# Kernel tuning notes

Measured on AMD Instinct MI355X. Metric: run time of the kernel, lower is better.

Reference implementation:

```python
import jax, jax.numpy as jnp
import numpy as np

NQ = 10
C64 = jnp.complex64

# ---- gate matrices (built from traced fp32 params) ----

def u3(t, p, d):
    c = jnp.cos(t * 0.5).astype(C64)
    s = jnp.sin(t * 0.5).astype(C64)
    ep = jnp.exp(1j * p.astype(C64))
    ed = jnp.exp(1j * d.astype(C64))
    return jnp.stack([jnp.stack([c, -ed * s]), jnp.stack([ep * s, ep * ed * c])])

def ry(t):
    c = jnp.cos(t * 0.5).astype(C64)
    s = jnp.sin(t * 0.5).astype(C64)
    return jnp.stack([jnp.stack([c, -s]), jnp.stack([s, c])])

def rz(t):
    e = jnp.exp(-0.5j * t.astype(C64))
    ep = jnp.exp(0.5j * t.astype(C64))
    return jnp.diag(jnp.stack([e, ep]))

def rx(t):
    c = jnp.cos(t * 0.5).astype(C64)
    s = jnp.sin(t * 0.5).astype(C64)
    return jnp.stack([jnp.stack([c, -1j * s]), jnp.stack([-1j * s, c])])

def crz(t):
    one = jnp.ones((), C64)
    return jnp.diag(jnp.stack([one, one, jnp.exp(-0.5j * t.astype(C64)), jnp.exp(0.5j * t.astype(C64))]))

def crx(t):
    return jnp.eye(4, dtype=C64).at[2:, 2:].set(rx(t))

X = jnp.array([[0, 1], [1, 0]], dtype=C64)
CNOT = jnp.array([[1, 0, 0, 0], [0, 1, 0, 0], [0, 0, 0, 1], [0, 0, 1, 0]], dtype=C64)

# ---- gate application on state of shape (B, 2,...,2) ----

def ap1(st, U, w):
    ax = 1 + w
    s = jnp.moveaxis(st, ax, -1)
    s = s @ U.T
    return jnp.moveaxis(s, -1, ax)

def ap2(st, U, a, b):
    s = jnp.moveaxis(st, (1 + a, 1 + b), (-2, -1))
    sh = s.shape
    s = s.reshape(sh[:-2] + (4,)) @ U.T
    return jnp.moveaxis(s.reshape(sh), (-2, -1), (1 + a, 1 + b))

def conv_block(st, w, a, b):
    st = ap1(st, u3(w[0], w[1], w[2]), a)
    st = ap1(st, u3(w[3], w[4], w[5]), b)
    st = ap2(st, CNOT, a, b)
    st = ap1(st, ry(w[6]), a)
    st = ap1(st, rz(w[7]), b)
    st = ap2(st, CNOT, b, a)
    st = ap1(st, ry(w[8]), a)
    st = ap2(st, CNOT, a, b)
    st = ap1(st, u3(w[9], w[10], w[11]), a)
    st = ap1(st, u3(w[12], w[13], w[14]), b)
    return st

def pool_block(st, p, c, t):
    st = ap2(st, crz(p[0]), c, t)
    st = ap1(st, X, c)
    st = ap2(st, crx(p[1]), c, t)
    return st

def zexp(st, w):
    p = jnp.abs(st) ** 2  # fp32
    axes = tuple(ax for ax in range(1, NQ + 1) if ax != 1 + w)
    pz = p.sum(axis=axes)  # (B, 2)
    return pz[:, 0] - pz[:, 1]


def setup_inputs() -> dict:
    key = jax.random.key(0)
    ks = jax.random.split(key, 6)
    two_pi = 2.0 * np.pi
    return {
        "x": jax.random.normal(ks[0], (16384, 1024), dtype=jnp.float32),
        "weights_conv1": jax.random.uniform(ks[1], (10, 15), jnp.float32) * two_pi,
        "weights_conv2": jax.random.uniform(ks[2], (4, 15), jnp.float32) * two_pi,
        "weights_pool1": jax.random.uniform(ks[3], (5, 2), jnp.float32) * two_pi,
        "weights_pool2": jax.random.uniform(ks[4], (2, 2), jnp.float32) * two_pi,
        "weights_fc": jax.random.uniform(ks[5], (3,), jnp.float32) * two_pi,
    }


def reference(x, weights_conv1, weights_conv2, weights_pool1, weights_pool2, weights_fc):
    B = x.shape[0]
    # AmplitudeEmbedding with normalize=True (input already 1024-dim, no padding)
    nrm = jnp.linalg.norm(x, axis=1, keepdims=True)
    st = (x / nrm).astype(C64).reshape((B,) + (2,) * NQ)
    # conv layer 1: even pairs, odd pairs, wraparound (0, 9) reusing row 7
    for i in range(0, NQ, 2):
        st = conv_block(st, weights_conv1[i], i, i + 1)
    for i in range(1, NQ - 1, 2):
        st = conv_block(st, weights_conv1[i], i, i + 1)
    st = conv_block(st, weights_conv1[7], 0, NQ - 1)
    # pool layer 1
    for idx, i in enumerate(range(0, NQ, 2)):
        st = pool_block(st, weights_pool1[idx], i + 1, i)
    # conv layer 2 (stride-2 wires)
    for idx, i in enumerate(range(0, NQ - 2, 2)):
        st = conv_block(st, weights_conv2[idx], i, i + 2)
    # pool layer 2
    for idx, i in enumerate(range(0, NQ - 2, 4)):
        st = pool_block(st, weights_pool2[idx], i + 2, i)
    # fully-connected entanglers + RX rotations
    st = ap2(st, CNOT, 0, 4)
    st = ap2(st, CNOT, 2, 4)
    st = ap2(st, CNOT, 4, 0)
    st = ap1(st, rx(weights_fc[0]), 0)
    st = ap1(st, rx(weights_fc[1]), 2)
    st = ap1(st, rx(weights_fc[2]), 4)
    return jnp.stack([zexp(st, 0), zexp(st, 2)], axis=-1)  # (B, 2)
```

## Files before the change

kernel.cpp:

```cpp
#include <hip/hip_runtime.h>


typedef _Float16 f16;
typedef f16 f16x8 __attribute__((ext_vector_type(8)));
typedef f16 f16x4 __attribute__((ext_vector_type(4)));
typedef f16 f16x2 __attribute__((ext_vector_type(2)));
typedef float f32x4 __attribute__((ext_vector_type(4)));

__device__ inline float2 cmul(float2 a, float2 b) {
    return make_float2(a.x * b.x - a.y * b.y, a.x * b.y + a.y * b.x);
}
__device__ inline float2 cadd(float2 a, float2 b) {
    return make_float2(a.x + b.x, a.y + b.y);
}

struct M2 { float2 m[4]; };

__device__ inline M2 m2_u3(float t, float p, float d) {
    float c = cosf(0.5f * t), s = sinf(0.5f * t);
    float2 ep = make_float2(cosf(p), sinf(p));
    float2 ed = make_float2(cosf(d), sinf(d));
    M2 U;
    U.m[0] = make_float2(c, 0.f);
    U.m[1] = make_float2(-ed.x * s, -ed.y * s);
    U.m[2] = make_float2(ep.x * s, ep.y * s);
    float2 epd = cmul(ep, ed);
    U.m[3] = make_float2(epd.x * c, epd.y * c);
    return U;
}
__device__ inline M2 m2_ry(float t) {
    float c = cosf(0.5f * t), s = sinf(0.5f * t);
    M2 U;
    U.m[0] = make_float2(c, 0.f);  U.m[1] = make_float2(-s, 0.f);
    U.m[2] = make_float2(s, 0.f);  U.m[3] = make_float2(c, 0.f);
    return U;
}
__device__ inline M2 m2_rz(float t) {
    float c = cosf(0.5f * t), s = sinf(0.5f * t);
    M2 U;
    U.m[0] = make_float2(c, -s); U.m[1] = make_float2(0.f, 0.f);
    U.m[2] = make_float2(0.f, 0.f); U.m[3] = make_float2(c, s);
    return U;
}
__device__ inline M2 m2_rx(float t) {
    float c = cosf(0.5f * t), s = sinf(0.5f * t);
    M2 U;
    U.m[0] = make_float2(c, 0.f);   U.m[1] = make_float2(0.f, -s);
    U.m[2] = make_float2(0.f, -s);  U.m[3] = make_float2(c, 0.f);
    return U;
}

__device__ inline void ap2x2(float2& x, float2& y, const M2& U) {
    float2 nx = cadd(cmul(U.m[0], x), cmul(U.m[1], y));
    float2 ny = cadd(cmul(U.m[2], x), cmul(U.m[3], y));
    x = nx; y = ny;
}
__device__ inline void apA(float2 v[4], const M2& U) { ap2x2(v[0], v[2], U); ap2x2(v[1], v[3], U); }
__device__ inline void apB(float2 v[4], const M2& U) { ap2x2(v[0], v[1], U); ap2x2(v[2], v[3], U); }
__device__ inline void swapv(float2& a, float2& b) { float2 t = a; a = b; b = t; }

__device__ inline void conv_col(const float* w, float2 v[4]) {
    apA(v, m2_u3(w[0], w[1], w[2]));
    apB(v, m2_u3(w[3], w[4], w[5]));
    swapv(v[2], v[3]);
    apA(v, m2_ry(w[6]));
    apB(v, m2_rz(w[7]));
    swapv(v[1], v[3]);
    apA(v, m2_ry(w[8]));
    swapv(v[2], v[3]);
    apA(v, m2_u3(w[9], w[10], w[11]));
    apB(v, m2_u3(w[12], w[13], w[14]));
}
__device__ inline void pool_col(const float* p, float2 v[4]) {
    {
        float c = cosf(0.5f * p[0]), s = sinf(0.5f * p[0]);
        v[2] = cmul(v[2], make_float2(c, -s));
        v[3] = cmul(v[3], make_float2(c, s));
    }
    swapv(v[0], v[2]); swapv(v[1], v[3]);
    {
        M2 U = m2_rx(p[1]);
        ap2x2(v[2], v[3], U);
    }
}

__global__ void build_gates(const float* wc1, const float* wc2,
                            const float* wp1, const float* wp2,
                            const float* wfc, int2* gp, float2* gm) {
    const int t = threadIdx.x;
    const int n = t >> 2, c = t & 3;
    if (blockIdx.x != 0 || n >= 27) return;

    float2 v[4];
    for (int i = 0; i < 4; i++) v[i] = make_float2(0.f, 0.f);
    v[c] = make_float2(1.f, 0.f);

    int a, b;
    if (n < 5)        { int i = 2*n;       a = i;   b = i+1; conv_col(wc1 + 15*i, v); }
    else if (n < 9)   { int i = 2*(n-5)+1; a = i;   b = i+1; conv_col(wc1 + 15*i, v); }
    else if (n == 9)  { a = 0; b = 9;      conv_col(wc1 + 105, v); }
    else if (n < 15)  { int idx = n-10, i = 2*idx; a = i+1; b = i; pool_col(wp1 + 2*idx, v); }
    else if (n < 19)  { int idx = n-15, i = 2*idx; a = i; b = i+2; conv_col(wc2 + 15*idx, v); }
    else if (n == 19) { a = 2; b = 0;      pool_col(wp2 + 0, v); }
    else if (n == 20) { a = 6; b = 4;      pool_col(wp2 + 2, v); }
    else if (n <= 23) {
        a = (n == 21) ? 0 : (n == 22) ? 2 : 4;
        b = (n == 23) ? 0 : 4;
        swapv(v[2], v[3]);
    } else {
        a = (n == 24) ? 0 : (n == 25) ? 2 : 4;
        b = a + 1;
        apA(v, m2_rx(wfc[n - 24]));
    }
    if (c == 0) gp[n] = make_int2(9 - a, 9 - b);
    for (int i = 0; i < 4; i++) gm[n * 16 + i * 4 + c] = v[i];
}

#define SIM_BLOCKS 512
#define NORM_BLOCKS 2048

__global__ __launch_bounds__(256) void prep(const float* __restrict__ X,
                                            const int2* __restrict__ gp,
                                            const float2* __restrict__ gm,
                                            float* __restrict__ nrm2,
                                            f16* __restrict__ Xh,
                                            f16* __restrict__ BTh,
                                            float* __restrict__ out) {
    __shared__ float2 st[2][1025];
    const int bid = blockIdx.x;

    if (bid >= SIM_BLOCKS) {
        const int nb = bid - SIM_BLOCKS;
        const int w = threadIdx.x >> 6, l = threadIdx.x & 63;
        if (threadIdx.x < 16) out[nb * 16 + threadIdx.x] = 1.0f;
#pragma unroll
        for (int r = 0; r < 2; r++) {
            const int row = nb * 8 + w * 2 + r;
            const float4* xr = (const float4*)(X + (size_t)row * 1024);
            float s = 0.f;
#pragma unroll
            for (int ch = 0; ch < 4; ch++) {
                float4 v = xr[ch * 64 + l];
                f16x4 h;
                h[0] = (f16)v.x; h[1] = (f16)v.y; h[2] = (f16)v.z; h[3] = (f16)v.w;
                *(f16x4*)(Xh + (size_t)row * 1024 + (ch * 64 + l) * 4) = h;
                s += v.x * v.x + v.y * v.y + v.z * v.z + v.w * v.w;
            }
#pragma unroll
            for (int off = 32; off >= 1; off >>= 1) s += __shfl_xor(s, off, 64);
            if (l == 0) nrm2[row] = s;
        }
        return;
    }

    const int sb = bid;
    const int t0 = (sb & 7) * 128 + (sb >> 3) * 2;

    for (int i = threadIdx.x; i < 1024; i += 256) {
        st[0][i] = make_float2((i == t0) ? 1.f : 0.f, 0.f);
        st[1][i] = make_float2((i == t0 + 1) ? 1.f : 0.f, 0.f);
    }
    __syncthreads();

    for (int g = 0; g < 27; g++) {
        const int2 p = gp[g];
        float2 m[16];
#pragma unroll
        for (int i = 0; i < 16; i++) m[i] = gm[g * 16 + i];
        const int p1 = p.x, p2 = p.y;
        const int lo = min(p1, p2), hi = max(p1, p2);
        const int q = threadIdx.x;
        const int m1 = (1 << lo) - 1;
        int tt = (q & m1) | ((q & ~m1) << 1);
        const int m2m = (1 << hi) - 1;
        const int i0 = (tt & m2m) | ((tt & ~m2m) << 1);
        int idx[4];
        for (int ga = 0; ga < 2; ga++)
            for (int gb = 0; gb < 2; gb++)
                idx[2 * ga + gb] = i0 | (ga << p1) | (gb << p2);
#pragma unroll
        for (int c = 0; c < 2; c++) {
            float2 v[4];
#pragma unroll
            for (int i = 0; i < 4; i++) v[i] = st[c][idx[i]];
#pragma unroll
            for (int i = 0; i < 4; i++) {
                float2 s = make_float2(0.f, 0.f);
#pragma unroll
                for (int j = 0; j < 4; j++) s = cadd(s, cmul(m[i * 4 + j], v[j]));
                st[c][idx[i]] = s;
            }
        }
        __syncthreads();
    }

    for (int s = threadIdx.x; s < 1024; s += 256) {
        const int b9 = (s >> 9) & 1, b7 = (s >> 7) & 1;
        if (b9 | b7) {
            const int grp = b9 ? b7 : 2;
            const int pos = (((s >> 8) & 1) << 7) | (s & 127);
            const int np = grp * 256 + pos;
            f16x2 re, im;
#pragma unroll
            for (int c = 0; c < 2; c++) {
                re[c] = (f16)st[c][s].x;
                im[c] = (f16)st[c][s].y;
            }
            *(f16x2*)(BTh + (size_t)np * 1024 + t0) = re;
            *(f16x2*)(BTh + (size_t)(np + 768) * 1024 + t0) = im;
        }
    }
}

__device__ __forceinline__ void glds16(const void* g, void* l) {
    __builtin_amdgcn_global_load_lds(
        (const __attribute__((address_space(1))) void*)g,
        (__attribute__((address_space(3))) void*)l, 16, 0, 0);
}

__global__ __launch_bounds__(512, 1) void gemm_mfma(const f16* __restrict__ A,
                                                    const f16* __restrict__ Bt,
                                                    const float* __restrict__ nrm2,
                                                    float* __restrict__ out) {
    __shared__ char lds[131072];
    const int tid = threadIdx.x;
    const int l = tid & 63, w = tid >> 6;
    const int wr = w >> 2, wc = w & 3;

    const int lin = blockIdx.x;
    const int xcd = lin & 7;
    const int mm = lin >> 3;
    const int rowT = xcd + 8 * (mm / 6);
    const int j = mm % 6;
    const int row0 = rowT * 256;
    const int col0 = j * 256;

    const int srow = l >> 3;
    const int kc = (l & 7) ^ (srow & 7);
    const f16* aS = A  + (size_t)(row0 + 32 * w + srow) * 1024 + kc * 8;
    const f16* bS = Bt + (size_t)(col0 + 32 * w + srow) * 1024 + kc * 8;

    int aOff[8][2], bOff[4][2];
#pragma unroll
    for (int h = 0; h < 2; h++) {
        const int cphys = (((l >> 4) + 4 * h) ^ (l & 7));
#pragma unroll
        for (int i = 0; i < 8; i++)
            aOff[i][h] = (wr * 128 + i * 16 + (l & 15)) * 128 + cphys * 16;
#pragma unroll
        for (int i = 0; i < 4; i++)
            bOff[i][h] = (wc * 64 + i * 16 + (l & 15)) * 128 + cphys * 16;
    }

    f32x4 acc[8][4];
    const f32x4 z = {0.f, 0.f, 0.f, 0.f};
#pragma unroll
    for (int i = 0; i < 8; i++)
#pragma unroll
        for (int n = 0; n < 4; n++) acc[i][n] = z;

    auto stage = [&](int t) {
        const int b = t & 1;
        char* aD = lds + b * 32768 + (32 * w) * 128;
        char* bD = lds + 65536 + b * 32768 + (32 * w) * 128;
#pragma unroll
        for (int g = 0; g < 4; ++g) {
            glds16(aS + t * 64 + g * 8 * 1024, aD + g * 1024);
            glds16(bS + t * 64 + g * 8 * 1024, bD + g * 1024);
        }
    };

    stage(0);
#pragma unroll 2
    for (int t = 0; t < 16; ++t) {
        asm volatile("s_waitcnt vmcnt(0)" ::: "memory");
        __builtin_amdgcn_s_barrier();
        if (t + 1 < 16) stage(t + 1);

        const char* aB = lds + (t & 1) * 32768;
        const char* bB = lds + 65536 + (t & 1) * 32768;
#pragma unroll
        for (int h = 0; h < 2; ++h) {
            f16x8 af[8], bf[4];
#pragma unroll
            for (int i = 0; i < 8; i++) af[i] = *(const f16x8*)(aB + aOff[i][h]);
#pragma unroll
            for (int i = 0; i < 4; i++) bf[i] = *(const f16x8*)(bB + bOff[i][h]);
            __builtin_amdgcn_s_setprio(1);
#pragma unroll
            for (int mi = 0; mi < 8; mi++)
#pragma unroll
                for (int ni = 0; ni < 4; ni++)
                    acc[mi][ni] = __builtin_amdgcn_mfma_f32_16x16x32_f16(
                        af[mi], bf[ni], acc[mi][ni], 0, 0, 0);
            __builtin_amdgcn_s_setprio(0);
        }
    }

    float c0[8][4], c1[8][4];
#pragma unroll
    for (int mi = 0; mi < 8; mi++)
#pragma unroll
        for (int rr = 0; rr < 4; rr++) { c0[mi][rr] = 0.f; c1[mi][rr] = 0.f; }
#pragma unroll
    for (int ni = 0; ni < 4; ni++) {
        const int n_glob = col0 + wc * 64 + ni * 16 + (l & 15);
        const int nm = (n_glob >= 768) ? n_glob - 768 : n_glob;
        const int grp = nm >> 8;
        const float w0 = (grp <= 1) ? 1.f : 0.f;
        const float w1 = (grp >= 1) ? 1.f : 0.f;
#pragma unroll
        for (int mi = 0; mi < 8; mi++)
#pragma unroll
            for (int rr = 0; rr < 4; rr++) {
                const float y = acc[mi][ni][rr];
                const float y2 = y * y;
                c0[mi][rr] += w0 * y2;
                c1[mi][rr] += w1 * y2;
            }
    }
#pragma unroll
    for (int off = 1; off < 16; off <<= 1)
#pragma unroll
        for (int mi = 0; mi < 8; mi++)
#pragma unroll
            for (int rr = 0; rr < 4; rr++) {
                c0[mi][rr] += __shfl_xor(c0[mi][rr], off, 64);
                c1[mi][rr] += __shfl_xor(c1[mi][rr], off, 64);
            }
    if ((l & 15) == 0) {
        const int q4 = l >> 4;
#pragma unroll
        for (int mi = 0; mi < 8; mi++)
#pragma unroll
            for (int rr = 0; rr < 4; rr++) {
                const int row = row0 + wr * 128 + mi * 16 + q4 * 4 + rr;
                const float inv = -2.0f / nrm2[row];
                atomicAdd(&out[row * 2 + 0], c0[mi][rr] * inv);
                atomicAdd(&out[row * 2 + 1], c1[mi][rr] * inv);
            }
    }
}

extern "C" void kernel_launch(void* const* d_in, const int* in_sizes, int n_in,
                              void* d_out, int out_size, void* d_ws, size_t ws_size,
                              hipStream_t stream) {
    const float* x   = (const float*)d_in[0];
    const float* wc1 = (const float*)d_in[1];
    const float* wc2 = (const float*)d_in[2];
    const float* wp1 = (const float*)d_in[3];
    const float* wp2 = (const float*)d_in[4];
    const float* wfc = (const float*)d_in[5];
    float* out = (float*)d_out;

    uintptr_t wsp = (uintptr_t)d_ws;
    int2*   gp     = (int2*)wsp;
    float2* gm     = (float2*)(wsp + 1024);
    f16*    BTh    = (f16*)(wsp + 8192);
    f16*    Xh     = (f16*)(wsp + 8192 + (3u << 20));
    float*  nrm2   = (float*)(wsp + 8192 + (35u << 20));

    build_gates<<<1, 128, 0, stream>>>(wc1, wc2, wp1, wp2, wfc, gp, gm);
    prep<<<SIM_BLOCKS + NORM_BLOCKS, 256, 0, stream>>>(x, gp, gm, nrm2, Xh, BTh, out);
    gemm_mfma<<<384, 512, 0, stream>>>(Xh, BTh, nrm2, out);
}
```

Measured before the change: 238.7 us.

## Restructure GEMM main loop into phased quadrant schedule with two blocks per CU

The GEMM inner loop is split into quadrant phases. Each phase loads a subset of A/B fragments from LDS, then issues a block of MFMAs, with s_barrier fences between phases and the global-to-LDS prefetch for the next K tile spread across them. This shrinks register fragments enough that launch_bounds can ask for 2 blocks per CU, so waves of different blocks overlap memory and math. Separately, the simulation part of prep handles 4 basis columns per block instead of 2, halving the sim block count and widening the stores. Risks include the many barriers, possible LDS limits on two 128KB blocks per CU, and register spills.

```diff
diff --git a/kernel.cpp b/kernel.cpp
--- a/kernel.cpp
+++ b/kernel.cpp
@@ -116,7 +116,7 @@
     for (int i = 0; i < 4; i++) gm[n * 16 + i * 4 + c] = v[i];
 }
 
-#define SIM_BLOCKS 512
+#define SIM_BLOCKS 256
 #define NORM_BLOCKS 2048
 
 __global__ __launch_bounds__(256) void prep(const float* __restrict__ X,
@@ -126,7 +126,7 @@
                                             f16* __restrict__ Xh,
                                             f16* __restrict__ BTh,
                                             float* __restrict__ out) {
-    __shared__ float2 st[2][1025];
+    __shared__ float2 st[4][1025];
     const int bid = blockIdx.x;
 
     if (bid >= SIM_BLOCKS) {
@@ -154,11 +154,12 @@
     }
 
     const int sb = bid;
-    const int t0 = (sb & 7) * 128 + (sb >> 3) * 2;
+    const int t0 = (sb & 7) * 128 + (sb >> 3) * 4;
 
     for (int i = threadIdx.x; i < 1024; i += 256) {
-        st[0][i] = make_float2((i == t0) ? 1.f : 0.f, 0.f);
-        st[1][i] = make_float2((i == t0 + 1) ? 1.f : 0.f, 0.f);
+#pragma unroll
+        for (int c = 0; c < 4; c++)
+            st[c][i] = make_float2((i == t0 + c) ? 1.f : 0.f, 0.f);
     }
     __syncthreads();
 
@@ -179,7 +180,7 @@
             for (int gb = 0; gb < 2; gb++)
                 idx[2 * ga + gb] = i0 | (ga << p1) | (gb << p2);
 #pragma unroll
-        for (int c = 0; c < 2; c++) {
+        for (int c = 0; c < 4; c++) {
             float2 v[4];
 #pragma unroll
             for (int i = 0; i < 4; i++) v[i] = st[c][idx[i]];
@@ -200,14 +201,14 @@
             const int grp = b9 ? b7 : 2;
             const int pos = (((s >> 8) & 1) << 7) | (s & 127);
             const int np = grp * 256 + pos;
-            f16x2 re, im;
-#pragma unroll
-            for (int c = 0; c < 2; c++) {
+            f16x4 re, im;
+#pragma unroll
+            for (int c = 0; c < 4; c++) {
                 re[c] = (f16)st[c][s].x;
                 im[c] = (f16)st[c][s].y;
             }
-            *(f16x2*)(BTh + (size_t)np * 1024 + t0) = re;
-            *(f16x2*)(BTh + (size_t)(np + 768) * 1024 + t0) = im;
+            *(f16x4*)(BTh + (size_t)np * 1024 + t0) = re;
+            *(f16x4*)(BTh + (size_t)(np + 768) * 1024 + t0) = im;
         }
     }
 }
@@ -218,7 +219,11 @@
         (__attribute__((address_space(3))) void*)l, 16, 0, 0);
 }
 
-__global__ __launch_bounds__(512, 1) void gemm_mfma(const f16* __restrict__ A,
+#define PH_BAR() do { __builtin_amdgcn_s_barrier(); \
+                      asm volatile("" ::: "memory"); } while (0)
+#define VM0()   asm volatile("s_waitcnt vmcnt(0)" ::: "memory")
+
+__global__ __launch_bounds__(512, 2) void gemm_mfma(const f16* __restrict__ A,
                                                     const f16* __restrict__ Bt,
                                                     const float* __restrict__ nrm2,
                                                     float* __restrict__ out) {
@@ -240,6 +245,19 @@
     const f16* aS = A  + (size_t)(row0 + 32 * w + srow) * 1024 + kc * 8;
     const f16* bS = Bt + (size_t)(col0 + 32 * w + srow) * 1024 + kc * 8;
 
+    auto stageA = [&](int t) {
+        char* aD = lds + (t & 1) * 32768 + (32 * w) * 128;
+#pragma unroll
+        for (int g = 0; g < 4; ++g)
+            glds16(aS + t * 64 + g * 8 * 1024, aD + g * 1024);
+    };
+    auto stageB = [&](int t) {
+        char* bD = lds + 65536 + (t & 1) * 32768 + (32 * w) * 128;
+#pragma unroll
+        for (int g = 0; g < 4; ++g)
+            glds16(bS + t * 64 + g * 8 * 1024, bD + g * 1024);
+    };
+
     int aOff[8][2], bOff[4][2];
 #pragma unroll
     for (int h = 0; h < 2; h++) {
@@ -259,43 +277,82 @@
 #pragma unroll
         for (int n = 0; n < 4; n++) acc[i][n] = z;
 
-    auto stage = [&](int t) {
-        const int b = t & 1;
-        char* aD = lds + b * 32768 + (32 * w) * 128;
-        char* bD = lds + 65536 + b * 32768 + (32 * w) * 128;
-#pragma unroll
-        for (int g = 0; g < 4; ++g) {
-            glds16(aS + t * 64 + g * 8 * 1024, aD + g * 1024);
-            glds16(bS + t * 64 + g * 8 * 1024, bD + g * 1024);
-        }
-    };
-
-    stage(0);
-#pragma unroll 2
-    for (int t = 0; t < 16; ++t) {
-        asm volatile("s_waitcnt vmcnt(0)" ::: "memory");
-        __builtin_amdgcn_s_barrier();
-        if (t + 1 < 16) stage(t + 1);
-
-        const char* aB = lds + (t & 1) * 32768;
-        const char* bB = lds + 65536 + (t & 1) * 32768;
-#pragma unroll
-        for (int h = 0; h < 2; ++h) {
-            f16x8 af[8], bf[4];
-#pragma unroll
-            for (int i = 0; i < 8; i++) af[i] = *(const f16x8*)(aB + aOff[i][h]);
-#pragma unroll
-            for (int i = 0; i < 4; i++) bf[i] = *(const f16x8*)(bB + bOff[i][h]);
-            __builtin_amdgcn_s_setprio(1);
-#pragma unroll
-            for (int mi = 0; mi < 8; mi++)
-#pragma unroll
-                for (int ni = 0; ni < 4; ni++)
-                    acc[mi][ni] = __builtin_amdgcn_mfma_f32_16x16x32_f16(
-                        af[mi], bf[ni], acc[mi][ni], 0, 0, 0);
-            __builtin_amdgcn_s_setprio(0);
-        }
-    }
+    f16x8 af[4][2], bf[2][2];
+
+#define READ_A(base, mb)                                                     \
+    _Pragma("unroll") for (int m_ = 0; m_ < 4; ++m_)                         \
+        _Pragma("unroll") for (int h_ = 0; h_ < 2; ++h_)                     \
+            af[m_][h_] = *(const f16x8*)((base) + aOff[(mb) + m_][h_]);
+#define READ_B(base, nb)                                                     \
+    _Pragma("unroll") for (int n_ = 0; n_ < 2; ++n_)                         \
+        _Pragma("unroll") for (int h_ = 0; h_ < 2; ++h_)                     \
+            bf[n_][h_] = *(const f16x8*)((base) + bOff[(nb) + n_][h_]);
+#define MFMA_Q(mb, nb) do {                                                  \
+    __builtin_amdgcn_s_setprio(1);                                           \
+    _Pragma("unroll") for (int h_ = 0; h_ < 2; ++h_)                         \
+        _Pragma("unroll") for (int m_ = 0; m_ < 4; ++m_)                     \
+            _Pragma("unroll") for (int n_ = 0; n_ < 2; ++n_)                 \
+                acc[(mb) + m_][(nb) + n_] =                                  \
+                    __builtin_amdgcn_mfma_f32_16x16x32_f16(                  \
+                        af[m_][h_], bf[n_][h_], acc[(mb) + m_][(nb) + n_],   \
+                        0, 0, 0);                                            \
+    __builtin_amdgcn_s_setprio(0); } while (0)
+
+    stageA(0); stageB(0);
+    VM0();
+    PH_BAR();
+
+    for (int i = 0; i < 8; ++i) {
+        const int t0 = 2 * i, t1 = 2 * i + 1;
+        const char* a0 = lds + (t0 & 1) * 32768;
+        const char* b0 = lds + 65536 + (t0 & 1) * 32768;
+        const char* a1 = lds + (t1 & 1) * 32768;
+        const char* b1 = lds + 65536 + (t1 & 1) * 32768;
+
+        READ_A(a0, 0); READ_B(b0, 0);
+        stageA(t1);
+        PH_BAR();
+        MFMA_Q(0, 0);
+        PH_BAR();
+        READ_A(a0, 4);
+        stageB(t1);
+        PH_BAR();
+        MFMA_Q(4, 0);
+        PH_BAR();
+        READ_B(b0, 2);
+        PH_BAR();
+        MFMA_Q(4, 2);
+        PH_BAR();
+        READ_A(a0, 0);
+        VM0();
+        PH_BAR();
+        MFMA_Q(0, 2);
+        PH_BAR();
+
+        READ_A(a1, 0); READ_B(b1, 0);
+        if (i < 7) stageA(t0 + 2);
+        PH_BAR();
+        MFMA_Q(0, 0);
+        PH_BAR();
+        READ_A(a1, 4);
+        if (i < 7) stageB(t0 + 2);
+        PH_BAR();
+        MFMA_Q(4, 0);
+        PH_BAR();
+        READ_B(b1, 2);
+        PH_BAR();
+        MFMA_Q(4, 2);
+        PH_BAR();
+        READ_A(a1, 0);
+        VM0();
+        PH_BAR();
+        MFMA_Q(0, 2);
+        PH_BAR();
+    }
+
+#undef READ_A
+#undef READ_B
+#undef MFMA_Q
 
     float c0[8][4], c1[8][4];
 #pragma unroll
```

Measured after the change: 254.4 us. 1.07x slower.
